# Kernel tuning notes

Measured on AMD Instinct MI355X. Metric: run time of the kernel, lower is better.

The kernel has to match this reference:

```python
import jax, jax.numpy as jnp
import numpy as np

B = 4          # batch_size (config.batch_size)
N = 17000      # num_prots (nodes per graph)
F_IN = 256     # num_features
C = 128        # out_channels
E = 2176000    # num edges (avg degree 32)
NODES = B * N


def _gcn_layer(x, W, b, src, dst, n):
    """PyG GCNConv: add self-loops, sym-normalized aggregation, then bias.
    out[i] = sum_{j->i} d_j^{-1/2} d_i^{-1/2} (x_j W) + d_i^{-1} (x_i W) + b
    with d = degree(dst) + 1 (self loop)."""
    h = x @ W  # [n, C]
    deg = jax.ops.segment_sum(jnp.ones(src.shape[0], x.dtype), dst, num_segments=n) + 1.0
    dinv = jax.lax.rsqrt(deg)  # [n]
    coef = dinv[src] * dinv[dst]                      # [E]
    agg = jax.ops.segment_sum(h[src] * coef[:, None], dst, num_segments=n)
    agg = agg + h * (dinv * dinv)[:, None]            # self-loop term
    return agg + b


def setup_inputs() -> dict:
    key = jax.random.key(0)
    ks = jax.random.split(key, 16)

    def glorot(k, shape):
        fan_in, fan_out = shape[0], shape[1]
        s = jnp.sqrt(6.0 / (fan_in + fan_out))
        return jax.random.uniform(k, shape, jnp.float32, -s, s)

    inp = {
        "x": jax.random.normal(ks[0], (NODES, F_IN), jnp.float32),
        "edge_index": jax.random.randint(ks[1], (2, E), 0, NODES, jnp.int32),
        "protein_mask": jax.random.randint(ks[2], (B, N), 0, 2, jnp.int32),
        "W1": glorot(ks[3], (F_IN, C)), "b1": jnp.zeros((C,), jnp.float32),
        "W2": glorot(ks[4], (C, C)),    "b2": jnp.zeros((C,), jnp.float32),
        "W3": glorot(ks[5], (C, C)),    "b3": jnp.zeros((C,), jnp.float32),
        "lw1": glorot(ks[6], (C, 256)), "lb1": jnp.zeros((256,), jnp.float32),
        "lw2": glorot(ks[7], (256, 64)), "lb2": jnp.zeros((64,), jnp.float32),
        "lw3": glorot(ks[8], (64, 16)),  "lb3": jnp.zeros((16,), jnp.float32),
        "lw4": glorot(ks[9], (16, 1)),   "lb4": jnp.zeros((1,), jnp.float32),
    }
    return inp


def reference(x, edge_index, protein_mask, W1, b1, W2, b2, W3, b3,
              lw1, lb1, lw2, lb2, lw3, lb3, lw4, lb4):
    src, dst = edge_index[0], edge_index[1]
    h1 = jax.nn.relu(_gcn_layer(x, W1, b1, src, dst, NODES))   # [NODES, C]
    h2 = jax.nn.relu(_gcn_layer(h1, W2, b2, src, dst, NODES))
    h3 = jax.nn.relu(_gcn_layer(h2, W3, b3, src, dst, NODES))
    s = (h1 + h2 + h3).reshape(B, N, C)                        # residual sum
    mask = protein_mask.astype(jnp.float32)                    # [B, N]
    pooled = jnp.einsum('bn,bnc->bc', mask, s)                 # masked bmm pool [B, C]
    z = jax.nn.relu(pooled @ lw1 + lb1)
    z = jax.nn.relu(z @ lw2 + lb2)
    z = jax.nn.relu(z @ lw3 + lb3)
    return z @ lw4 + lb4                                       # [B, 1]
```

## Files before the change

kernel.cpp:

```cpp
#include <hip/hip_runtime.h>
#include <hip/hip_bf16.h>
#include <cstdint>

#define F_IN 256
#define C 128
#define NBUK_MAX 320
#define CHUNK 4096
#define CAP 12288

typedef short bf8_t __attribute__((ext_vector_type(8)));
typedef float f4_t  __attribute__((ext_vector_type(4)));

static inline size_t align256(size_t x) { return (x + 255) & ~(size_t)255; }


__global__ __launch_bounds__(256) void partition_kernel(const int* __restrict__ src,
                                                        const int* __restrict__ dst,
                                                        int* __restrict__ cntb,
                                                        int* __restrict__ ebuf, int E) {
    __shared__ int hist[NBUK_MAX];
    __shared__ int base[NBUK_MAX];
    __shared__ int gbase[NBUK_MAX];
    __shared__ int2 stage[CHUNK];
    const int tid = threadIdx.x;
    const int e0 = blockIdx.x * CHUNK;
    const int cnt = min(CHUNK, E - e0);

    for (int i = tid; i < NBUK_MAX; i += 256) hist[i] = 0;
    __syncthreads();

    int2 ev[CHUNK / 256];
    int mo[CHUNK / 256];
#pragma unroll
    for (int k = 0; k < CHUNK / 256; ++k) {
        int e = e0 + k * 256 + tid;
        if (e < E) {
            int2 v;
            v.x = src[e];
            v.y = dst[e];
            ev[k] = v;
            mo[k] = atomicAdd(&hist[v.y >> 8], 1);
        }
    }
    __syncthreads();
    if (tid < 64) {
        int acc[5];
        int s = 0;
#pragma unroll
        for (int j = 0; j < 5; ++j) {
            int idx = tid * 5 + j;
            acc[j] = s;
            s += hist[idx];
        }
        int tot = s;
#pragma unroll
        for (int d = 1; d < 64; d <<= 1) {
            int o = __shfl_up(tot, d);
            if (tid >= d) tot += o;
        }
        int excl = tot - s;
#pragma unroll
        for (int j = 0; j < 5; ++j) base[tid * 5 + j] = excl + acc[j];
    }
    __syncthreads();
    for (int i = tid; i < NBUK_MAX; i += 256) {
        int h = hist[i];
        gbase[i] = h ? atomicAdd(&cntb[i], h) : 0;
    }
    __syncthreads();
#pragma unroll
    for (int k = 0; k < CHUNK / 256; ++k) {
        int e = e0 + k * 256 + tid;
        if (e < E) stage[base[ev[k].y >> 8] + mo[k]] = ev[k];
    }
    __syncthreads();
    for (int i = tid; i < cnt; i += 256) {
        int2 e = stage[i];
        int b = e.y >> 8;
        ebuf[(size_t)b * CAP + gbase[b] + (i - base[b])] = ((e.y & 255) << 24) | e.x;
    }
}

__global__ __launch_bounds__(256) void bscan_kernel(const int* __restrict__ cntb,
                                                    int nbuk,
                                                    int* __restrict__ ebase) {
    __shared__ int sums[NBUK_MAX];
    __shared__ int base[NBUK_MAX + 1];
    const int tid = threadIdx.x;
    for (int bk = tid; bk < NBUK_MAX; bk += 256)
        sums[bk] = (bk < nbuk) ? cntb[bk] : 0;
    __syncthreads();
    if (tid < 64) {
        int acc[5];
        int s = 0;
#pragma unroll
        for (int j = 0; j < 5; ++j) {
            acc[j] = s;
            s += sums[tid * 5 + j];
        }
        int tot = s;
#pragma unroll
        for (int d = 1; d < 64; d <<= 1) {
            int o = __shfl_up(tot, d);
            if (tid >= d) tot += o;
        }
        int excl = tot - s;
#pragma unroll
        for (int j = 0; j < 5; ++j) base[tid * 5 + j] = excl + acc[j];
        if (tid == 63) base[320] = tot;
    }
    __syncthreads();
    for (int bk = tid; bk <= nbuk; bk += 256)
        ebase[bk] = base[bk];
}

__global__ __launch_bounds__(256) void csr_build_kernel(const int* __restrict__ ebuf,
                                                        const int* __restrict__ ebase,
                                                        int* __restrict__ offs,
                                                        float* __restrict__ dinv,
                                                        int* __restrict__ csr, int nodes) {
    __shared__ int deg[256];
    __shared__ int p[256];
    __shared__ int pre[257];
    __shared__ int cur[256];
    const int b = blockIdx.x;
    const int n0 = b << 8;
    const int ncnt = min(256, nodes - n0);
    const int tid = threadIdx.x;
    const int eb = ebase[b];
    const int cntE = ebase[b + 1] - eb;
    const int* slab = ebuf + (size_t)b * CAP;

    deg[tid] = 0;
    __syncthreads();
    for (int k = tid; k < cntE; k += 256)
        atomicAdd(&deg[(unsigned)slab[k] >> 24], 1);
    __syncthreads();
    p[tid] = deg[tid];
    __syncthreads();
    for (int d = 1; d < 256; d <<= 1) {
        int v = (tid >= d) ? p[tid - d] : 0;
        __syncthreads();
        p[tid] += v;
        __syncthreads();
    }
    pre[tid + 1] = p[tid];
    if (tid == 0) pre[0] = 0;
    __syncthreads();

    for (int i = tid; i <= ncnt; i += 256)
        offs[n0 + i] = eb + pre[i] + n0 + i;
    if (tid < ncnt) {
        dinv[n0 + tid] = rsqrtf((float)(deg[tid] + 1));
        csr[eb + pre[tid] + n0 + tid] = n0 + tid;
    }
    cur[tid] = 0;
    __syncthreads();
    for (int k = tid; k < cntE; k += 256) {
        int v = slab[k];
        int loc = (unsigned)v >> 24;
        int q = atomicAdd(&cur[loc], 1);
        csr[eb + pre[loc] + n0 + loc + 1 + q] = v & 0xFFFFFF;
    }
}

static __device__ inline unsigned pack_bf16(float a, float b) {
    __hip_bfloat162 h = __float22bfloat162_rn(make_float2(a, b));
    return *(unsigned*)&h;
}

static __device__ inline void swz_one(const float* __restrict__ W,
                                      __hip_bfloat16* __restrict__ Wsw, int i) {
    int l = i & 63;
    int u = (i >> 6) & 7;
    int t = i >> 9;
    int krow = t * 32 + (l >> 4) * 8;
    int col = u * 16 + (l & 15);
    unsigned packed[4];
#pragma unroll
    for (int j = 0; j < 4; ++j) {
        float a = W[(size_t)(krow + 2 * j) * C + col];
        float b = W[(size_t)(krow + 2 * j + 1) * C + col];
        packed[j] = pack_bf16(a, b);
    }
    uint4 o = make_uint4(packed[0], packed[1], packed[2], packed[3]);
    *(uint4*)(Wsw + (size_t)i * 8) = o;
}

__global__ __launch_bounds__(256) void wswz_all_kernel(const float* __restrict__ W1,
                                                       const float* __restrict__ W2,
                                                       const float* __restrict__ W3,
                                                       __hip_bfloat16* __restrict__ Wsw1,
                                                       __hip_bfloat16* __restrict__ Wsw2,
                                                       __hip_bfloat16* __restrict__ Wsw3) {
    int i = blockIdx.x * blockDim.x + threadIdx.x;
    if (i < 4096)      swz_one(W1, Wsw1, i);
    else if (i < 6144) swz_one(W2, Wsw2, i - 4096);
    else if (i < 8192) swz_one(W3, Wsw3, i - 6144);
}


static __device__ inline bf8_t pack8(float4 u0, float4 u1) {
    union { unsigned u[4]; bf8_t v; } r;
    r.u[0] = pack_bf16(u0.x, u0.y);
    r.u[1] = pack_bf16(u0.z, u0.w);
    r.u[2] = pack_bf16(u1.x, u1.y);
    r.u[3] = pack_bf16(u1.z, u1.w);
    return r.v;
}

template <bool F32IN>
__global__ __launch_bounds__(256) void mfma_gemm_kernel(const void* __restrict__ Xv,
                                                        const __hip_bfloat16* __restrict__ Wsw,
                                                        const float* __restrict__ dinv,
                                                        __hip_bfloat16* __restrict__ G,
                                                        int M, int K) {
    __shared__ char lds[32768];
    const int tid = threadIdx.x;
    const int l = tid & 63;
    const int w = tid >> 6;
    const int lm = l & 15;
    const int lk = (l >> 4) * 8;
    const int row0 = blockIdx.x * 128 + w * 32;

    f4_t acc[2][8] = {};
    const int steps = K >> 5;

    const float* xf[2];
    const __hip_bfloat16* xb[2];
#pragma unroll
    for (int mt = 0; mt < 2; ++mt) {
        int r = min(row0 + mt * 16 + lm, M - 1);
        xf[mt] = (const float*)Xv + (size_t)r * K + lk;
        xb[mt] = (const __hip_bfloat16*)Xv + (size_t)r * K + lk;
    }

    float4 cf[2][2];
    bf8_t cb[2];
#pragma unroll
    for (int mt = 0; mt < 2; ++mt) {
        if (F32IN) {
            cf[mt][0] = *(const float4*)(xf[mt]);
            cf[mt][1] = *(const float4*)(xf[mt] + 4);
        } else {
            cb[mt] = *(const bf8_t*)(xb[mt]);
        }
    }

    for (int s = 0; s < steps; ++s) {
        if ((s & 3) == 0) {
            if (s) __syncthreads();
            const char* wsrc = (const char*)Wsw + (size_t)s * 8192;
            for (int o = tid * 16; o < 32768; o += 256 * 16)
                *(uint4*)(lds + o) = *(const uint4*)(wsrc + o);
            __syncthreads();
        }
        float4 nf[2][2];
        bf8_t nb[2];
        if (s + 1 < steps) {
#pragma unroll
            for (int mt = 0; mt < 2; ++mt) {
                if (F32IN) {
                    nf[mt][0] = *(const float4*)(xf[mt] + (s + 1) * 32);
                    nf[mt][1] = *(const float4*)(xf[mt] + (s + 1) * 32 + 4);
                } else {
                    nb[mt] = *(const bf8_t*)(xb[mt] + (s + 1) * 32);
                }
            }
        }
        bf8_t a[2];
#pragma unroll
        for (int mt = 0; mt < 2; ++mt)
            a[mt] = F32IN ? pack8(cf[mt][0], cf[mt][1]) : cb[mt];

        const char* bbase = lds + ((size_t)((s & 3) * 8) * 64 + l) * 16;
#pragma unroll
        for (int u = 0; u < 8; ++u) {
            bf8_t b = *(const bf8_t*)(bbase + (size_t)u * 64 * 16);
#pragma unroll
            for (int mt = 0; mt < 2; ++mt)
                acc[mt][u] = __builtin_amdgcn_mfma_f32_16x16x32_bf16(a[mt], b, acc[mt][u], 0, 0, 0);
        }
#pragma unroll
        for (int mt = 0; mt < 2; ++mt) {
            if (F32IN) {
                cf[mt][0] = nf[mt][0];
                cf[mt][1] = nf[mt][1];
            } else {
                cb[mt] = nb[mt];
            }
        }
    }

#pragma unroll
    for (int mt = 0; mt < 2; ++mt) {
        int rbase = row0 + mt * 16 + (l >> 4) * 4;
#pragma unroll
        for (int r = 0; r < 4; ++r) {
            int row = rbase + r;
            if (row < M) {
                float dv = dinv[row];
#pragma unroll
                for (int u = 0; u < 8; ++u) {
                    float v = acc[mt][u][r] * dv;
                    G[(size_t)row * C + u * 16 + lm] = __float2bfloat16(v);
                }
            }
        }
    }
}

static __device__ inline void unpack_add(uint4 v, float* acc) {
    const __hip_bfloat162* hh = (const __hip_bfloat162*)&v;
#pragma unroll
    for (int t = 0; t < 4; ++t) {
        float2 f = __bfloat1622float2(hh[t]);
        acc[2 * t]     += f.x;
        acc[2 * t + 1] += f.y;
    }
}

static __device__ inline void gather_rows(const char* __restrict__ Gb,
                                          const int* __restrict__ csr,
                                          int beg, int end, int l, int g,
                                          unsigned qoff, float* acc) {
    for (int base = beg; base < end; base += 64) {
        const int cnt = min(64, end - base);
        int myidx = (l < cnt) ? csr[base + l] : 0;
        int j = 0;
        for (; j + 16 <= cnt; j += 16) {
            int i0 = __shfl(myidx, j + g);
            int i1 = __shfl(myidx, j + 4 + g);
            int i2 = __shfl(myidx, j + 8 + g);
            int i3 = __shfl(myidx, j + 12 + g);
            uint4 v0 = *(const uint4*)(Gb + (((unsigned)i0 << 8) | qoff));
            uint4 v1 = *(const uint4*)(Gb + (((unsigned)i1 << 8) | qoff));
            uint4 v2 = *(const uint4*)(Gb + (((unsigned)i2 << 8) | qoff));
            uint4 v3 = *(const uint4*)(Gb + (((unsigned)i3 << 8) | qoff));
            unpack_add(v0, acc); unpack_add(v1, acc);
            unpack_add(v2, acc); unpack_add(v3, acc);
        }
        if (j + 8 <= cnt) {
            int i0 = __shfl(myidx, j + g);
            int i1 = __shfl(myidx, j + 4 + g);
            uint4 v0 = *(const uint4*)(Gb + (((unsigned)i0 << 8) | qoff));
            uint4 v1 = *(const uint4*)(Gb + (((unsigned)i1 << 8) | qoff));
            unpack_add(v0, acc); unpack_add(v1, acc);
            j += 8;
        }
        for (; j < cnt; j += 4) {
            int i0 = __shfl(myidx, j + g);
            float sc = (j + g < cnt) ? 1.f : 0.f;
            uint4 v0 = *(const uint4*)(Gb + (((unsigned)i0 << 8) | qoff));
            const __hip_bfloat162* h0 = (const __hip_bfloat162*)&v0;
#pragma unroll
            for (int t = 0; t < 4; ++t) {
                float2 f0 = __bfloat1622float2(h0[t]);
                acc[2 * t]     = fmaf(f0.x, sc, acc[2 * t]);
                acc[2 * t + 1] = fmaf(f0.y, sc, acc[2 * t + 1]);
            }
        }
    }
}

__global__ __launch_bounds__(256) void agg_kernel(const __hip_bfloat16* __restrict__ G,
                                                  const int* __restrict__ csr,
                                                  const int* __restrict__ offs,
                                                  const float* __restrict__ dinv,
                                                  const float* __restrict__ bias,
                                                  __hip_bfloat16* __restrict__ A, int nodes) {
    const int node = blockIdx.x * 4 + (threadIdx.x >> 6);
    if (node >= nodes) return;
    const int l = threadIdx.x & 63;
    const int g = l >> 4;
    const unsigned qoff = (l & 15) * 16;
    const int beg = offs[node], end = offs[node + 1];
    float acc[8] = {};
    gather_rows((const char*)G, csr, beg, end, l, g, qoff, acc);

#pragma unroll
    for (int t = 0; t < 8; ++t) {
        acc[t] += __shfl_xor(acc[t], 16);
        acc[t] += __shfl_xor(acc[t], 32);
    }

    const float d = dinv[node];
    if (g == 0) {
        float bb[8];
        *(float4*)bb       = *(const float4*)(bias + qoff / 2);
        *(float4*)(bb + 4) = *(const float4*)(bias + qoff / 2 + 4);
        unsigned pk[4];
#pragma unroll
        for (int t = 0; t < 4; ++t) {
            float x0 = fmaxf(fmaf(acc[2 * t],     d, bb[2 * t]),     0.f);
            float x1 = fmaxf(fmaf(acc[2 * t + 1], d, bb[2 * t + 1]), 0.f);
            pk[t] = pack_bf16(x0, x1);
        }
        *(uint4*)((char*)A + (size_t)node * 256 + qoff) = make_uint4(pk[0], pk[1], pk[2], pk[3]);
    }
}

__global__ __launch_bounds__(64) void pool3_kernel(const __hip_bfloat16* __restrict__ S1,
                                                   const __hip_bfloat16* __restrict__ S2,
                                                   const __hip_bfloat16* __restrict__ S3,
                                                   const int* __restrict__ mask,
                                                   float* __restrict__ pooled, int N) {
    const int b = blockIdx.y;
    const int n0 = blockIdx.x * 128;
    const int c0 = threadIdx.x * 2;
    const int lim = min(n0 + 128, N);
    float ax = 0.f, ay = 0.f;
    for (int n = n0; n < lim; ++n) {
        if (mask[b * N + n]) {
            size_t o = ((size_t)b * N + n) * C + c0;
            float2 f1 = __bfloat1622float2(*(const __hip_bfloat162*)(S1 + o));
            float2 f2 = __bfloat1622float2(*(const __hip_bfloat162*)(S2 + o));
            float2 f3 = __bfloat1622float2(*(const __hip_bfloat162*)(S3 + o));
            ax += f1.x + f2.x + f3.x;
            ay += f1.y + f2.y + f3.y;
        }
    }
    atomicAdd(&pooled[b * C + c0], ax);
    atomicAdd(&pooled[b * C + c0 + 1], ay);
}

__global__ __launch_bounds__(256) void mlp_kernel(const float* __restrict__ pooled,
        const float* __restrict__ lw1, const float* __restrict__ lb1,
        const float* __restrict__ lw2, const float* __restrict__ lb2,
        const float* __restrict__ lw3, const float* __restrict__ lb3,
        const float* __restrict__ lw4, const float* __restrict__ lb4,
        float* __restrict__ out) {
    __shared__ float p[4 * 128];
    __shared__ float z1[4 * 256];
    __shared__ float z2[4 * 64];
    __shared__ float z3[4 * 16];
    const int tid = threadIdx.x;
    for (int i = tid; i < 4 * 128; i += 256) p[i] = pooled[i];
    __syncthreads();
    for (int o = tid; o < 4 * 256; o += 256) {
        int b = o >> 8, j = o & 255;
        float s = lb1[j];
        for (int k = 0; k < 128; ++k) s += p[b * 128 + k] * lw1[k * 256 + j];
        z1[o] = fmaxf(s, 0.f);
    }
    __syncthreads();
    for (int o = tid; o < 4 * 64; o += 256) {
        int b = o >> 6, j = o & 63;
        float s = lb2[j];
        for (int k = 0; k < 256; ++k) s += z1[b * 256 + k] * lw2[k * 64 + j];
        z2[o] = fmaxf(s, 0.f);
    }
    __syncthreads();
    if (tid < 64) {
        int b = tid >> 4, j = tid & 15;
        float s = lb3[j];
        for (int k = 0; k < 64; ++k) s += z2[b * 64 + k] * lw3[k * 16 + j];
        z3[tid] = fmaxf(s, 0.f);
    }
    __syncthreads();
    if (tid < 4) {
        float s = lb4[0];
        for (int k = 0; k < 16; ++k) s += z3[tid * 16 + k] * lw4[k];
        out[tid] = s;
    }
}


extern "C" void kernel_launch(void* const* d_in, const int* in_sizes, int n_in,
                              void* d_out, int out_size, void* d_ws, size_t ws_size,
                              hipStream_t stream) {
    const float* x    = (const float*)d_in[0];
    const int*   ei   = (const int*)d_in[1];
    const int*   pmask = (const int*)d_in[2];
    const float* W1 = (const float*)d_in[3];  const float* b1 = (const float*)d_in[4];
    const float* W2 = (const float*)d_in[5];  const float* b2 = (const float*)d_in[6];
    const float* W3 = (const float*)d_in[7];  const float* b3 = (const float*)d_in[8];
    const float* lw1 = (const float*)d_in[9];  const float* lb1 = (const float*)d_in[10];
    const float* lw2 = (const float*)d_in[11]; const float* lb2 = (const float*)d_in[12];
    const float* lw3 = (const float*)d_in[13]; const float* lb3 = (const float*)d_in[14];
    const float* lw4 = (const float*)d_in[15]; const float* lb4 = (const float*)d_in[16];
    float* out = (float*)d_out;

    const int E = in_sizes[1] / 2;
    const int NODES = in_sizes[0] / F_IN;
    const int NB = 4;
    const int NPER = NODES / NB;
    const int NBUK = (NODES + 255) >> 8;
    const int NBLK = (E + CHUNK - 1) / CHUNK;
    const int* esrc = ei;
    const int* edst = ei + E;

    char* w = (char*)d_ws;
    size_t off = 0;
    auto alloc = [&](size_t bytes) -> void* {
        void* p = w + off;
        off = align256(off + bytes);
        return p;
    };
    float* dinv = (float*)alloc((size_t)NODES * 4);
    int*   offs = (int*)  alloc((size_t)(NODES + 1) * 4);
    int*   ebase = (int*) alloc((size_t)(NBUK + 1) * 4);
    int*   cntb = (int*)  alloc((size_t)NBUK * 4);
    int*   ebuf = (int*)  alloc((size_t)NBUK * CAP * 4);
    int*   csr  = (int*)  alloc((size_t)(E + NODES) * 4);
    __hip_bfloat16* G   = (__hip_bfloat16*)alloc((size_t)NODES * C * 2);
    __hip_bfloat16* A1  = (__hip_bfloat16*)alloc((size_t)NODES * C * 2);
    __hip_bfloat16* A2  = (__hip_bfloat16*)alloc((size_t)NODES * C * 2);
    __hip_bfloat16* A3  = (__hip_bfloat16*)alloc((size_t)NODES * C * 2);
    __hip_bfloat16* Wsw1 = (__hip_bfloat16*)alloc((size_t)F_IN * C * 2);
    __hip_bfloat16* Wsw2 = (__hip_bfloat16*)alloc((size_t)C * C * 2);
    __hip_bfloat16* Wsw3 = (__hip_bfloat16*)alloc((size_t)C * C * 2);
    float* pooled = (float*)alloc((size_t)4 * C * 4);
    (void)ws_size; (void)n_in; (void)out_size;

    hipMemsetAsync(cntb,   0, (size_t)NBUK * 4, stream);
    hipMemsetAsync(pooled, 0, (size_t)4 * C * 4, stream);

    wswz_all_kernel<<<32, 256, 0, stream>>>(W1, W2, W3, Wsw1, Wsw2, Wsw3);

    partition_kernel<<<NBLK, 256, 0, stream>>>(esrc, edst, cntb, ebuf, E);
    bscan_kernel<<<1, 256, 0, stream>>>(cntb, NBUK, ebase);
    csr_build_kernel<<<NBUK, 256, 0, stream>>>(ebuf, ebase, offs, dinv, csr, NODES);

    const int gblocks128 = (NODES + 127) / 128;
    const int ablocks = (NODES + 3) / 4;

    mfma_gemm_kernel<true><<<gblocks128, 256, 0, stream>>>(x, Wsw1, dinv, G, NODES, F_IN);
    agg_kernel<<<ablocks, 256, 0, stream>>>(G, csr, offs, dinv, b1, A1, NODES);
    mfma_gemm_kernel<false><<<gblocks128, 256, 0, stream>>>(A1, Wsw2, dinv, G, NODES, C);
    agg_kernel<<<ablocks, 256, 0, stream>>>(G, csr, offs, dinv, b2, A2, NODES);
    mfma_gemm_kernel<false><<<gblocks128, 256, 0, stream>>>(A2, Wsw3, dinv, G, NODES, C);
    agg_kernel<<<ablocks, 256, 0, stream>>>(G, csr, offs, dinv, b3, A3, NODES);

    dim3 pgrid((NPER + 127) / 128, NB);
    pool3_kernel<<<pgrid, 64, 0, stream>>>(A1, A2, A3, pmask, pooled, NPER);
    mlp_kernel<<<1, 256, 0, stream>>>(pooled, lw1, lb1, lw2, lb2, lw3, lb3, lw4, lb4, out);
}
```

Before: 481.9 us.

## Fuse edge partition with first GEMM and fold bucket scan into CSR build

Edge partitioning and the layer-1 feature GEMM now run in one launch, with block ranges split between the two independent jobs so they overlap. The GEMM no longer needs dinv, so the source-side normalization for layer 1 moves into the aggregation gather as a per-neighbor dinv scale. The separate bucket-scan kernel is removed: each CSR-build block redoes the small prefix scan locally. This cuts launches and serialization at the cost of redundant scans and extra dinv loads in the first aggregation.

```diff
diff --git a/kernel.cpp b/kernel.cpp
--- a/kernel.cpp
+++ b/kernel.cpp
@@ -13,112 +13,169 @@
 
 static inline size_t align256(size_t x) { return (x + 255) & ~(size_t)255; }
 
-
-__global__ __launch_bounds__(256) void partition_kernel(const int* __restrict__ src,
-                                                        const int* __restrict__ dst,
-                                                        int* __restrict__ cntb,
-                                                        int* __restrict__ ebuf, int E) {
-    __shared__ int hist[NBUK_MAX];
-    __shared__ int base[NBUK_MAX];
-    __shared__ int gbase[NBUK_MAX];
-    __shared__ int2 stage[CHUNK];
+static __device__ inline unsigned pack_bf16(float a, float b) {
+    __hip_bfloat162 h = __float22bfloat162_rn(make_float2(a, b));
+    return *(unsigned*)&h;
+}
+
+static __device__ inline bf8_t pack8(float4 u0, float4 u1) {
+    union { unsigned u[4]; bf8_t v; } r;
+    r.u[0] = pack_bf16(u0.x, u0.y);
+    r.u[1] = pack_bf16(u0.z, u0.w);
+    r.u[2] = pack_bf16(u1.x, u1.y);
+    r.u[3] = pack_bf16(u1.z, u1.w);
+    return r.v;
+}
+
+__global__ __launch_bounds__(256) void part_gemm1_kernel(
+        const int* __restrict__ src, const int* __restrict__ dst,
+        int* __restrict__ cntb, int* __restrict__ ebuf, int E, int nblk_part,
+        const float* __restrict__ X, const __hip_bfloat16* __restrict__ Wsw,
+        __hip_bfloat16* __restrict__ G, int M) {
+    __shared__ __align__(16) char smem[36864];
     const int tid = threadIdx.x;
-    const int e0 = blockIdx.x * CHUNK;
-    const int cnt = min(CHUNK, E - e0);
-
-    for (int i = tid; i < NBUK_MAX; i += 256) hist[i] = 0;
-    __syncthreads();
-
-    int2 ev[CHUNK / 256];
-    int mo[CHUNK / 256];
-#pragma unroll
-    for (int k = 0; k < CHUNK / 256; ++k) {
-        int e = e0 + k * 256 + tid;
-        if (e < E) {
-            int2 v;
-            v.x = src[e];
-            v.y = dst[e];
-            ev[k] = v;
-            mo[k] = atomicAdd(&hist[v.y >> 8], 1);
-        }
-    }
-    __syncthreads();
-    if (tid < 64) {
-        int acc[5];
-        int s = 0;
-#pragma unroll
-        for (int j = 0; j < 5; ++j) {
-            int idx = tid * 5 + j;
-            acc[j] = s;
-            s += hist[idx];
-        }
-        int tot = s;
-#pragma unroll
-        for (int d = 1; d < 64; d <<= 1) {
-            int o = __shfl_up(tot, d);
-            if (tid >= d) tot += o;
-        }
-        int excl = tot - s;
-#pragma unroll
-        for (int j = 0; j < 5; ++j) base[tid * 5 + j] = excl + acc[j];
-    }
-    __syncthreads();
-    for (int i = tid; i < NBUK_MAX; i += 256) {
-        int h = hist[i];
-        gbase[i] = h ? atomicAdd(&cntb[i], h) : 0;
-    }
-    __syncthreads();
-#pragma unroll
-    for (int k = 0; k < CHUNK / 256; ++k) {
-        int e = e0 + k * 256 + tid;
-        if (e < E) stage[base[ev[k].y >> 8] + mo[k]] = ev[k];
-    }
-    __syncthreads();
-    for (int i = tid; i < cnt; i += 256) {
-        int2 e = stage[i];
-        int b = e.y >> 8;
-        ebuf[(size_t)b * CAP + gbase[b] + (i - base[b])] = ((e.y & 255) << 24) | e.x;
-    }
-}
-
-__global__ __launch_bounds__(256) void bscan_kernel(const int* __restrict__ cntb,
-                                                    int nbuk,
-                                                    int* __restrict__ ebase) {
-    __shared__ int sums[NBUK_MAX];
-    __shared__ int base[NBUK_MAX + 1];
-    const int tid = threadIdx.x;
-    for (int bk = tid; bk < NBUK_MAX; bk += 256)
-        sums[bk] = (bk < nbuk) ? cntb[bk] : 0;
-    __syncthreads();
-    if (tid < 64) {
-        int acc[5];
-        int s = 0;
-#pragma unroll
-        for (int j = 0; j < 5; ++j) {
-            acc[j] = s;
-            s += sums[tid * 5 + j];
-        }
-        int tot = s;
-#pragma unroll
-        for (int d = 1; d < 64; d <<= 1) {
-            int o = __shfl_up(tot, d);
-            if (tid >= d) tot += o;
-        }
-        int excl = tot - s;
-#pragma unroll
-        for (int j = 0; j < 5; ++j) base[tid * 5 + j] = excl + acc[j];
-        if (tid == 63) base[320] = tot;
-    }
-    __syncthreads();
-    for (int bk = tid; bk <= nbuk; bk += 256)
-        ebase[bk] = base[bk];
+
+    if ((int)blockIdx.x < nblk_part) {
+        int* hist = (int*)smem;
+        int* base = hist + NBUK_MAX;
+        int* gbase = base + NBUK_MAX;
+        int2* stage = (int2*)(smem + 4096);
+        const int e0 = blockIdx.x * CHUNK;
+        const int cnt = min(CHUNK, E - e0);
+
+        for (int i = tid; i < NBUK_MAX; i += 256) hist[i] = 0;
+        __syncthreads();
+
+        int2 ev[CHUNK / 256];
+        int mo[CHUNK / 256];
+#pragma unroll
+        for (int k = 0; k < CHUNK / 256; ++k) {
+            int e = e0 + k * 256 + tid;
+            if (e < E) {
+                int2 v;
+                v.x = src[e];
+                v.y = dst[e];
+                ev[k] = v;
+                mo[k] = atomicAdd(&hist[v.y >> 8], 1);
+            }
+        }
+        __syncthreads();
+        if (tid < 64) {
+            int acc[5];
+            int s = 0;
+#pragma unroll
+            for (int j = 0; j < 5; ++j) {
+                acc[j] = s;
+                s += hist[tid * 5 + j];
+            }
+            int tot = s;
+#pragma unroll
+            for (int d = 1; d < 64; d <<= 1) {
+                int o = __shfl_up(tot, d);
+                if (tid >= d) tot += o;
+            }
+            int excl = tot - s;
+#pragma unroll
+            for (int j = 0; j < 5; ++j) base[tid * 5 + j] = excl + acc[j];
+        }
+        __syncthreads();
+        for (int i = tid; i < NBUK_MAX; i += 256) {
+            int h = hist[i];
+            gbase[i] = h ? atomicAdd(&cntb[i], h) : 0;
+        }
+        __syncthreads();
+#pragma unroll
+        for (int k = 0; k < CHUNK / 256; ++k) {
+            int e = e0 + k * 256 + tid;
+            if (e < E) stage[base[ev[k].y >> 8] + mo[k]] = ev[k];
+        }
+        __syncthreads();
+        for (int i = tid; i < cnt; i += 256) {
+            int2 e = stage[i];
+            int b = e.y >> 8;
+            ebuf[(size_t)b * CAP + gbase[b] + (i - base[b])] = ((e.y & 255) << 24) | e.x;
+        }
+    } else {
+        char* lds = smem;
+        const int gb = blockIdx.x - nblk_part;
+        const int l = tid & 63;
+        const int w = tid >> 6;
+        const int lm = l & 15;
+        const int lk = (l >> 4) * 8;
+        const int row0 = gb * 128 + w * 32;
+        const int K = F_IN;
+
+        f4_t acc[2][8] = {};
+        const float* xf[2];
+#pragma unroll
+        for (int mt = 0; mt < 2; ++mt) {
+            int r = min(row0 + mt * 16 + lm, M - 1);
+            xf[mt] = X + (size_t)r * K + lk;
+        }
+        float4 cf[2][2];
+#pragma unroll
+        for (int mt = 0; mt < 2; ++mt) {
+            cf[mt][0] = *(const float4*)(xf[mt]);
+            cf[mt][1] = *(const float4*)(xf[mt] + 4);
+        }
+        for (int s = 0; s < 8; ++s) {
+            if ((s & 3) == 0) {
+                if (s) __syncthreads();
+                const char* wsrc = (const char*)Wsw + (size_t)s * 8192;
+                for (int o = tid * 16; o < 32768; o += 256 * 16)
+                    *(uint4*)(lds + o) = *(const uint4*)(wsrc + o);
+                __syncthreads();
+            }
+            float4 nf[2][2];
+            if (s + 1 < 8) {
+#pragma unroll
+                for (int mt = 0; mt < 2; ++mt) {
+                    nf[mt][0] = *(const float4*)(xf[mt] + (s + 1) * 32);
+                    nf[mt][1] = *(const float4*)(xf[mt] + (s + 1) * 32 + 4);
+                }
+            }
+            bf8_t a[2];
+#pragma unroll
+            for (int mt = 0; mt < 2; ++mt)
+                a[mt] = pack8(cf[mt][0], cf[mt][1]);
+            const char* bbase = lds + ((size_t)((s & 3) * 8) * 64 + l) * 16;
+#pragma unroll
+            for (int u = 0; u < 8; ++u) {
+                bf8_t b = *(const bf8_t*)(bbase + (size_t)u * 64 * 16);
+#pragma unroll
+                for (int mt = 0; mt < 2; ++mt)
+                    acc[mt][u] = __builtin_amdgcn_mfma_f32_16x16x32_bf16(a[mt], b, acc[mt][u], 0, 0, 0);
+            }
+#pragma unroll
+            for (int mt = 0; mt < 2; ++mt) {
+                cf[mt][0] = nf[mt][0];
+                cf[mt][1] = nf[mt][1];
+            }
+        }
+#pragma unroll
+        for (int mt = 0; mt < 2; ++mt) {
+            int rbase = row0 + mt * 16 + (l >> 4) * 4;
+#pragma unroll
+            for (int r = 0; r < 4; ++r) {
+                int row = rbase + r;
+                if (row < M) {
+#pragma unroll
+                    for (int u = 0; u < 8; ++u)
+                        G[(size_t)row * C + u * 16 + lm] = __float2bfloat16(acc[mt][u][r]);
+                }
+            }
+        }
+    }
 }
 
 __global__ __launch_bounds__(256) void csr_build_kernel(const int* __restrict__ ebuf,
-                                                        const int* __restrict__ ebase,
+                                                        const int* __restrict__ cntb,
+                                                        int nbuk,
                                                         int* __restrict__ offs,
                                                         float* __restrict__ dinv,
                                                         int* __restrict__ csr, int nodes) {
+    __shared__ int hist[NBUK_MAX];
+    __shared__ int basep[NBUK_MAX];
     __shared__ int deg[256];
     __shared__ int p[256];
     __shared__ int pre[257];
@@ -127,8 +184,31 @@
     const int n0 = b << 8;
     const int ncnt = min(256, nodes - n0);
     const int tid = threadIdx.x;
-    const int eb = ebase[b];
-    const int cntE = ebase[b + 1] - eb;
+
+    for (int bk = tid; bk < NBUK_MAX; bk += 256)
+        hist[bk] = (bk < nbuk) ? cntb[bk] : 0;
+    __syncthreads();
+    if (tid < 64) {
+        int acc[5];
+        int s = 0;
+#pragma unroll
+        for (int j = 0; j < 5; ++j) {
+            acc[j] = s;
+            s += hist[tid * 5 + j];
+        }
+        int tot = s;
+#pragma unroll
+        for (int d = 1; d < 64; d <<= 1) {
+            int o = __shfl_up(tot, d);
+            if (tid >= d) tot += o;
+        }
+        int excl = tot - s;
+#pragma unroll
+        for (int j = 0; j < 5; ++j) basep[tid * 5 + j] = excl + acc[j];
+    }
+    __syncthreads();
+    const int eb = basep[b];
+    const int cntE = hist[b];
     const int* slab = ebuf + (size_t)b * CAP;
 
     deg[tid] = 0;
@@ -162,11 +242,6 @@
         int q = atomicAdd(&cur[loc], 1);
         csr[eb + pre[loc] + n0 + loc + 1 + q] = v & 0xFFFFFF;
     }
-}
-
-static __device__ inline unsigned pack_bf16(float a, float b) {
-    __hip_bfloat162 h = __float22bfloat162_rn(make_float2(a, b));
-    return *(unsigned*)&h;
 }
 
 static __device__ inline void swz_one(const float* __restrict__ W,
@@ -199,22 +274,11 @@
     else if (i < 8192) swz_one(W3, Wsw3, i - 6144);
 }
 
-
-static __device__ inline bf8_t pack8(float4 u0, float4 u1) {
-    union { unsigned u[4]; bf8_t v; } r;
-    r.u[0] = pack_bf16(u0.x, u0.y);
-    r.u[1] = pack_bf16(u0.z, u0.w);
-    r.u[2] = pack_bf16(u1.x, u1.y);
-    r.u[3] = pack_bf16(u1.z, u1.w);
-    return r.v;
-}
-
-template <bool F32IN>
-__global__ __launch_bounds__(256) void mfma_gemm_kernel(const void* __restrict__ Xv,
+__global__ __launch_bounds__(256) void mfma_gemm_kernel(const __hip_bfloat16* __restrict__ Xv,
                                                         const __hip_bfloat16* __restrict__ Wsw,
                                                         const float* __restrict__ dinv,
                                                         __hip_bfloat16* __restrict__ G,
-                                                        int M, int K) {
+                                                        int M) {
     __shared__ char lds[32768];
     const int tid = threadIdx.x;
     const int l = tid & 63;
@@ -222,74 +286,42 @@
     const int lm = l & 15;
     const int lk = (l >> 4) * 8;
     const int row0 = blockIdx.x * 128 + w * 32;
+    const int K = C;
 
     f4_t acc[2][8] = {};
-    const int steps = K >> 5;
-
-    const float* xf[2];
     const __hip_bfloat16* xb[2];
 #pragma unroll
     for (int mt = 0; mt < 2; ++mt) {
         int r = min(row0 + mt * 16 + lm, M - 1);
-        xf[mt] = (const float*)Xv + (size_t)r * K + lk;
-        xb[mt] = (const __hip_bfloat16*)Xv + (size_t)r * K + lk;
-    }
-
-    float4 cf[2][2];
+        xb[mt] = Xv + (size_t)r * K + lk;
+    }
     bf8_t cb[2];
 #pragma unroll
-    for (int mt = 0; mt < 2; ++mt) {
-        if (F32IN) {
-            cf[mt][0] = *(const float4*)(xf[mt]);
-            cf[mt][1] = *(const float4*)(xf[mt] + 4);
-        } else {
-            cb[mt] = *(const bf8_t*)(xb[mt]);
-        }
-    }
-
-    for (int s = 0; s < steps; ++s) {
-        if ((s & 3) == 0) {
-            if (s) __syncthreads();
-            const char* wsrc = (const char*)Wsw + (size_t)s * 8192;
-            for (int o = tid * 16; o < 32768; o += 256 * 16)
-                *(uint4*)(lds + o) = *(const uint4*)(wsrc + o);
-            __syncthreads();
-        }
-        float4 nf[2][2];
+    for (int mt = 0; mt < 2; ++mt)
+        cb[mt] = *(const bf8_t*)(xb[mt]);
+
+    for (int o = tid * 16; o < 32768; o += 256 * 16)
+        *(uint4*)(lds + o) = *(const uint4*)((const char*)Wsw + o);
+    __syncthreads();
+
+    for (int s = 0; s < 4; ++s) {
         bf8_t nb[2];
-        if (s + 1 < steps) {
-#pragma unroll
-            for (int mt = 0; mt < 2; ++mt) {
-                if (F32IN) {
-                    nf[mt][0] = *(const float4*)(xf[mt] + (s + 1) * 32);
-                    nf[mt][1] = *(const float4*)(xf[mt] + (s + 1) * 32 + 4);
-                } else {
-                    nb[mt] = *(const bf8_t*)(xb[mt] + (s + 1) * 32);
-                }
-            }
-        }
-        bf8_t a[2];
-#pragma unroll
-        for (int mt = 0; mt < 2; ++mt)
-            a[mt] = F32IN ? pack8(cf[mt][0], cf[mt][1]) : cb[mt];
-
-        const char* bbase = lds + ((size_t)((s & 3) * 8) * 64 + l) * 16;
+        if (s + 1 < 4) {
+#pragma unroll
+            for (int mt = 0; mt < 2; ++mt)
+                nb[mt] = *(const bf8_t*)(xb[mt] + (s + 1) * 32);
+        }
+        const char* bbase = lds + ((size_t)(s * 8) * 64 + l) * 16;
 #pragma unroll
         for (int u = 0; u < 8; ++u) {
             bf8_t b = *(const bf8_t*)(bbase + (size_t)u * 64 * 16);
 #pragma unroll
             for (int mt = 0; mt < 2; ++mt)
-                acc[mt][u] = __builtin_amdgcn_mfma_f32_16x16x32_bf16(a[mt], b, acc[mt][u], 0, 0, 0);
-        }
-#pragma unroll
-        for (int mt = 0; mt < 2; ++mt) {
-            if (F32IN) {
-                cf[mt][0] = nf[mt][0];
-                cf[mt][1] = nf[mt][1];
-            } else {
-                cb[mt] = nb[mt];
-            }
-        }
+                acc[mt][u] = __builtin_amdgcn_mfma_f32_16x16x32_bf16(cb[mt], b, acc[mt][u], 0, 0, 0);
+        }
+#pragma unroll
+        for (int mt = 0; mt < 2; ++mt)
+            cb[mt] = nb[mt];
     }
 
 #pragma unroll
@@ -320,13 +352,26 @@
     }
 }
 
+static __device__ inline void unpack_fma(uint4 v, float dv, float* acc) {
+    const __hip_bfloat162* hh = (const __hip_bfloat162*)&v;
+#pragma unroll
+    for (int t = 0; t < 4; ++t) {
+        float2 f = __bfloat1622float2(hh[t]);
+        acc[2 * t]     = fmaf(f.x, dv, acc[2 * t]);
+        acc[2 * t + 1] = fmaf(f.y, dv, acc[2 * t + 1]);
+    }
+}
+
+template <bool SS>
 static __device__ inline void gather_rows(const char* __restrict__ Gb,
                                           const int* __restrict__ csr,
+                                          const float* __restrict__ dinv,
                                           int beg, int end, int l, int g,
                                           unsigned qoff, float* acc) {
     for (int base = beg; base < end; base += 64) {
         const int cnt = min(64, end - base);
         int myidx = (l < cnt) ? csr[base + l] : 0;
+        float mydv = SS ? dinv[myidx] : 1.f;
         int j = 0;
         for (; j + 16 <= cnt; j += 16) {
             int i0 = __shfl(myidx, j + g);
@@ -337,32 +382,43 @@
             uint4 v1 = *(const uint4*)(Gb + (((unsigned)i1 << 8) | qoff));
             uint4 v2 = *(const uint4*)(Gb + (((unsigned)i2 << 8) | qoff));
             uint4 v3 = *(const uint4*)(Gb + (((unsigned)i3 << 8) | qoff));
-            unpack_add(v0, acc); unpack_add(v1, acc);
-            unpack_add(v2, acc); unpack_add(v3, acc);
+            if (SS) {
+                float d0 = __shfl(mydv, j + g);
+                float d1 = __shfl(mydv, j + 4 + g);
+                float d2 = __shfl(mydv, j + 8 + g);
+                float d3 = __shfl(mydv, j + 12 + g);
+                unpack_fma(v0, d0, acc); unpack_fma(v1, d1, acc);
+                unpack_fma(v2, d2, acc); unpack_fma(v3, d3, acc);
+            } else {
+                unpack_add(v0, acc); unpack_add(v1, acc);
+                unpack_add(v2, acc); unpack_add(v3, acc);
+            }
         }
         if (j + 8 <= cnt) {
             int i0 = __shfl(myidx, j + g);
             int i1 = __shfl(myidx, j + 4 + g);
             uint4 v0 = *(const uint4*)(Gb + (((unsigned)i0 << 8) | qoff));
             uint4 v1 = *(const uint4*)(Gb + (((unsigned)i1 << 8) | qoff));
-            unpack_add(v0, acc); unpack_add(v1, acc);
+            if (SS) {
+                float d0 = __shfl(mydv, j + g);
+                float d1 = __shfl(mydv, j + 4 + g);
+                unpack_fma(v0, d0, acc); unpack_fma(v1, d1, acc);
+            } else {
+                unpack_add(v0, acc); unpack_add(v1, acc);
+            }
             j += 8;
         }
         for (; j < cnt; j += 4) {
             int i0 = __shfl(myidx, j + g);
             float sc = (j + g < cnt) ? 1.f : 0.f;
+            if (SS) sc *= __shfl(mydv, j + g);
             uint4 v0 = *(const uint4*)(Gb + (((unsigned)i0 << 8) | qoff));
-            const __hip_bfloat162* h0 = (const __hip_bfloat162*)&v0;
-#pragma unroll
-            for (int t = 0; t < 4; ++t) {
-                float2 f0 = __bfloat1622float2(h0[t]);
-                acc[2 * t]     = fmaf(f0.x, sc, acc[2 * t]);
-                acc[2 * t + 1] = fmaf(f0.y, sc, acc[2 * t + 1]);
-            }
-        }
-    }
-}
-
+            unpack_fma(v0, sc, acc);
+        }
+    }
+}
+
+template <bool SS>
 __global__ __launch_bounds__(256) void agg_kernel(const __hip_bfloat16* __restrict__ G,
                                                   const int* __restrict__ csr,
                                                   const int* __restrict__ offs,
@@ -376,7 +432,7 @@
     const unsigned qoff = (l & 15) * 16;
     const int beg = offs[node], end = offs[node + 1];
     float acc[8] = {};
-    gather_rows((const char*)G, csr, beg, end, l, g, qoff, acc);
+    gather_rows<SS>((const char*)G, csr, dinv, beg, end, l, g, qoff, acc);
 
 #pragma unroll
     for (int t = 0; t < 8; ++t) {
@@ -499,7 +555,6 @@
     };
     float* dinv = (float*)alloc((size_t)NODES * 4);
     int*   offs = (int*)  alloc((size_t)(NODES + 1) * 4);
-    int*   ebase = (int*) alloc((size_t)(NBUK + 1) * 4);
     int*   cntb = (int*)  alloc((size_t)NBUK * 4);
     int*   ebuf = (int*)  alloc((size_t)NBUK * CAP * 4);
     int*   csr  = (int*)  alloc((size_t)(E + NODES) * 4);
@@ -516,21 +571,21 @@
     hipMemsetAsync(cntb,   0, (size_t)NBUK * 4, stream);
     hipMemsetAsync(pooled, 0, (size_t)4 * C * 4, stream);
 
-    wswz_all_kernel<<<32, 256, 0, stream>>>(W1, W2, W3, Wsw1, Wsw2, Wsw3);
-
-    partition_kernel<<<NBLK, 256, 0, stream>>>(esrc, edst, cntb, ebuf, E);
-    bscan_kernel<<<1, 256, 0, stream>>>(cntb, NBUK, ebase);
-    csr_build_kernel<<<NBUK, 256, 0, stream>>>(ebuf, ebase, offs, dinv, csr, NODES);
-
     const int gblocks128 = (NODES + 127) / 128;
     const int ablocks = (NODES + 3) / 4;
 
-    mfma_gemm_kernel<true><<<gblocks128, 256, 0, stream>>>(x, Wsw1, dinv, G, NODES, F_IN);
-    agg_kernel<<<ablocks, 256, 0, stream>>>(G, csr, offs, dinv, b1, A1, NODES);
-    mfma_gemm_kernel<false><<<gblocks128, 256, 0, stream>>>(A1, Wsw2, dinv, G, NODES, C);
-    agg_kernel<<<ablocks, 256, 0, stream>>>(G, csr, offs, dinv, b2, A2, NODES);
-    mfma_gemm_kernel<false><<<gblocks128, 256, 0, stream>>>(A2, Wsw3, dinv, G, NODES, C);
-    agg_kernel<<<ablocks, 256, 0, stream>>>(G, csr, offs, dinv, b3, A3, NODES);
+    wswz_all_kernel<<<32, 256, 0, stream>>>(W1, W2, W3, Wsw1, Wsw2, Wsw3);
+
+    part_gemm1_kernel<<<NBLK + gblocks128, 256, 0, stream>>>(
+        esrc, edst, cntb, ebuf, E, NBLK, x, Wsw1, G, NODES);
+
+    csr_build_kernel<<<NBUK, 256, 0, stream>>>(ebuf, cntb, NBUK, offs, dinv, csr, NODES);
+
+    agg_kernel<true><<<ablocks, 256, 0, stream>>>(G, csr, offs, dinv, b1, A1, NODES);
+    mfma_gemm_kernel<<<gblocks128, 256, 0, stream>>>(A1, Wsw2, dinv, G, NODES);
+    agg_kernel<false><<<ablocks, 256, 0, stream>>>(G, csr, offs, dinv, b2, A2, NODES);
+    mfma_gemm_kernel<<<gblocks128, 256, 0, stream>>>(A2, Wsw3, dinv, G, NODES);
+    agg_kernel<false><<<ablocks, 256, 0, stream>>>(G, csr, offs, dinv, b3, A3, NODES);
 
     dim3 pgrid((NPER + 127) / 128, NB);
     pool3_kernel<<<pgrid, 64, 0, stream>>>(A1, A2, A3, pmask, pooled, NPER);
```

After: 480.0 us. No clear change (-0.4%).
